# Kernel tuning notes

Measured on AMD Instinct MI355X. Metric: run time of the kernel, lower is better.

The kernel has to match this reference:

```python
import jax, jax.numpy as jnp
import numpy as np

N, E = 25000, 400000
NIN, NOUT, HID = 32, 32, 128


def setup_inputs() -> dict:
    key = jax.random.key(0)
    ks = jax.random.split(key, 8)
    s = lambda d: 1.0 / np.sqrt(d)
    return {
        "x": jax.random.normal(ks[0], (N, NIN), jnp.float32),
        "edge_index": jax.random.randint(ks[1], (2, E), 0, N, jnp.int64),
        "edge_attr": jax.random.normal(ks[2], (E, NIN), jnp.float32),
        # edge-MLP: Linear(NIN,HID) -> ReLU -> Linear(HID, NIN*NOUT)
        "w1": jax.random.normal(ks[3], (NIN, HID), jnp.float32) * s(NIN),
        "b1": jnp.zeros((HID,), jnp.float32),
        "w2": jax.random.normal(ks[4], (HID, NIN * NOUT), jnp.float32) * s(HID),
        "b2": jnp.zeros((NIN * NOUT,), jnp.float32),
        # NNConv root weight and bias
        "root": jax.random.normal(ks[5], (NIN, NOUT), jnp.float32) * s(NIN),
        "bias": jnp.zeros((NOUT,), jnp.float32),
    }


def reference(x, edge_index, edge_attr, w1, b1, w2, b2, root, bias):
    src, dst = edge_index[0], edge_index[1]
    # per-edge weight matrices from edge-attr MLP: [E, NIN, NOUT]
    h = jax.nn.relu(edge_attr @ w1 + b1)
    W = (h @ w2 + b2).reshape(-1, NIN, NOUT)
    # gather source features, per-edge small matmul: [E, NOUT]
    msg = jnp.einsum("ei,eio->eo", x[src], W)
    # scatter-add to target nodes (PyG default aggr='add')
    agg = jax.ops.segment_sum(msg, dst, num_segments=N)
    # root/self transform + bias
    return agg + x @ root + bias
```

## Files before the change

### kernel.cpp

```cpp
#include <hip/hip_runtime.h>
#include <hip/hip_fp16.h>


#define NN 25000
#define EE 400000

typedef _Float16 f16x8 __attribute__((ext_vector_type(8)));
typedef float    f32x16 __attribute__((ext_vector_type(16)));

__global__ __launch_bounds__(256) void prep_final_kernel(
    const float* __restrict__ x, const float* __restrict__ root,
    const float* __restrict__ bias,
    const float* __restrict__ w1, const float* __restrict__ w2,
    const float* __restrict__ b2,
    _Float16* __restrict__ w2p, _Float16* __restrict__ w1p, _Float16* __restrict__ b2p,
    float* __restrict__ out)
{
    const int t = blockIdx.x * 256 + threadIdx.x;

    if (t < 131072) {
        int j = t & 7, lane = (t >> 3) & 63, ih = (t >> 9) & 1, c = t >> 10;
        w2p[t] = (_Float16)w2[c * 1024 + (ih * 16 + ((lane >> 5) << 3) + j) * 32 + (lane & 31)];
    } else if (t < 135168) {
        int u = t - 131072;
        int j = u & 7, lane = (u >> 3) & 63, kk = (u >> 9) & 1, r = u >> 10;
        w1p[u] = (_Float16)w1[(kk * 16 + ((lane >> 5) << 3) + j) * 128 + r * 32 + (lane & 31)];
    } else if (t < 136192) {
        int u = t - 135168;
        int j = u & 7, lane = (u >> 3) & 63, ih = u >> 9;
        b2p[u] = (_Float16)b2[(ih * 16 + ((lane >> 5) << 3) + j) * 32 + (lane & 31)];
    }

    int n = t >> 5, o = t & 31;
    float acc = bias[o];
    const float* xr = x + (n << 5);
#pragma unroll
    for (int i = 0; i < 32; ++i)
        acc = fmaf(xr[i], root[(i << 5) + o], acc);
    out[t] = acc;
}

__global__ __launch_bounds__(128, 2) void edge_kernel(
    const float*    __restrict__ x,
    const int*      __restrict__ ei,
    const float*    __restrict__ ea,
    const float*    __restrict__ b1,
    const _Float16* __restrict__ w2p,
    const _Float16* __restrict__ w1p,
    const _Float16* __restrict__ b2p,
    float* __restrict__ out)
{
    __shared__ unsigned short hTq[2][32][32][4];

    const int t    = threadIdx.x;
    const int w    = t >> 6;
    const int lane = t & 63;
    const int l    = lane & 31;
    const int half = lane >> 5;

    const int  ebraw = blockIdx.x * 256 + w * 128;
    const bool live  = (ebraw + 128) <= EE;
    const int  ebw   = live ? ebraw : (EE - 128);

    union u8h { f16x8 v; __half2 h2[4]; };

    const f16x8* __restrict__ w2f = (const f16x8*)w2p;

    f16x8 BA[2], BB[2], BC[2], BD[2];
    auto loadCol = [&](int j, f16x8 (&B)[2]) {
        const f16x8* p = w2f + (size_t)j * 128 + lane;
        B[0] = p[0];
        B[1] = p[64];
    };
    loadCol(0, BA); loadCol(1, BB); loadCol(2, BC); loadCol(3, BD);

    u8h eaf[4][2];
#pragma unroll
    for (int g = 0; g < 4; ++g)
#pragma unroll
        for (int kk = 0; kk < 2; ++kk) {
            const float* p = ea + (size_t)(ebw + g * 32 + l) * 32 + kk * 16 + half * 8;
            float4 a0 = *(const float4*)p;
            float4 a1 = *(const float4*)(p + 4);
            eaf[g][kk].h2[0] = __float22half2_rn(make_float2(a0.x, a0.y));
            eaf[g][kk].h2[1] = __float22half2_rn(make_float2(a0.z, a0.w));
            eaf[g][kk].h2[2] = __float22half2_rn(make_float2(a1.x, a1.y));
            eaf[g][kk].h2[3] = __float22half2_rn(make_float2(a1.z, a1.w));
        }

    __half2 xs[4][8];
#pragma unroll
    for (int g = 0; g < 4; ++g) {
        int s = ei[ebw + g * 32 + l];
#pragma unroll
        for (int ih = 0; ih < 2; ++ih) {
            float4 a0 = *(const float4*)(x + s * 32 + ih * 16 + half * 8);
            float4 a1 = *(const float4*)(x + s * 32 + ih * 16 + half * 8 + 4);
            xs[g][ih*4+0] = __float22half2_rn(make_float2(a0.x, a0.y));
            xs[g][ih*4+1] = __float22half2_rn(make_float2(a0.z, a0.w));
            xs[g][ih*4+2] = __float22half2_rn(make_float2(a1.x, a1.y));
            xs[g][ih*4+3] = __float22half2_rn(make_float2(a1.z, a1.w));
        }
    }

    f32x16 acc[4];
#pragma unroll
    for (int g = 0; g < 4; ++g)
#pragma unroll
        for (int i = 0; i < 16; ++i) acc[g][i] = 0.f;

    auto phase1 = [&](int r) {
        f16x8 w1f0 = *(const f16x8*)(w1p + ((r * 2 + 0) * 64 + lane) * 8);
        f16x8 w1f1 = *(const f16x8*)(w1p + ((r * 2 + 1) * 64 + lane) * 8);
#pragma unroll
        for (int g = 0; g < 4; ++g) {
            f32x16 h;
#pragma unroll
            for (int i = 0; i < 16; ++i) h[i] = 0.f;
            h = __builtin_amdgcn_mfma_f32_32x32x16_f16(w1f0, eaf[g][0].v, h, 0, 0, 0);
            h = __builtin_amdgcn_mfma_f32_32x32x16_f16(w1f1, eaf[g][1].v, h, 0, 0, 0);
#pragma unroll
            for (int i = 0; i < 16; ++i) {
                int row = (i & 3) + ((i >> 2) << 3) + (half << 2);
                float hv = fmaxf(h[i] + b1[r * 32 + row], 0.f);
                hTq[w][row][l][g] = __half_as_ushort(__float2half(hv));
            }
        }
    };

    auto computeCol = [&](int cs, const f16x8 (&B)[2]) {
        uint2 u = *(const uint2*)&hTq[w][cs][l][0];
        __half2 ha = *reinterpret_cast<const __half2*>(&u.x);
        __half2 hb = *reinterpret_cast<const __half2*>(&u.y);
        __half2 d[4];
        d[0] = __half2half2(__low2half(ha));
        d[1] = __half2half2(__high2half(ha));
        d[2] = __half2half2(__low2half(hb));
        d[3] = __half2half2(__high2half(hb));
#pragma unroll
        for (int ih = 0; ih < 2; ++ih) {
            f16x8 bfr = B[ih];
#pragma unroll
            for (int g = 0; g < 4; ++g) {
                u8h A;
#pragma unroll
                for (int p = 0; p < 4; ++p)
                    A.h2[p] = __hmul2(d[g], xs[g][ih * 4 + p]);
                acc[g] = __builtin_amdgcn_mfma_f32_32x32x16_f16(A.v, bfr, acc[g], 0, 0, 0);
            }
        }
    };

#pragma unroll 1
    for (int r = 0; r < 4; ++r) {
        phase1(r);
#pragma unroll 1
        for (int q = 0; q < 8; ++q) {
            const int j = r * 32 + q * 4;
            computeCol(q * 4 + 0, BA); loadCol(j + 4, BA);
            computeCol(q * 4 + 1, BB); loadCol(j + 5, BB);
            computeCol(q * 4 + 2, BC); loadCol(j + 6, BC);
            computeCol(q * 4 + 3, BD); loadCol(j + 7, BD);
        }
    }

#pragma unroll
    for (int ih = 0; ih < 2; ++ih) {
        f16x8 bfr = *(const f16x8*)(b2p + (ih * 64 + lane) * 8);
#pragma unroll
        for (int g = 0; g < 4; ++g) {
            u8h A;
#pragma unroll
            for (int p = 0; p < 4; ++p) A.h2[p] = xs[g][ih * 4 + p];
            acc[g] = __builtin_amdgcn_mfma_f32_32x32x16_f16(A.v, bfr, acc[g], 0, 0, 0);
        }
    }

    if (live) {
#pragma unroll
        for (int g = 0; g < 4; ++g)
#pragma unroll
            for (int i = 0; i < 16; ++i) {
                int el = (i & 3) + ((i >> 2) << 3) + (half << 2);
                atomicAdd(out + (size_t)ei[EE + ebw + g * 32 + el] * 32 + l, acc[g][i]);
            }
    }
}

extern "C" void kernel_launch(void* const* d_in, const int* in_sizes, int n_in,
                              void* d_out, int out_size, void* d_ws, size_t ws_size,
                              hipStream_t stream) {
    const float* x    = (const float*)d_in[0];
    const int*   ei   = (const int*)  d_in[1];
    const float* ea   = (const float*)d_in[2];
    const float* w1   = (const float*)d_in[3];
    const float* b1   = (const float*)d_in[4];
    const float* w2   = (const float*)d_in[5];
    const float* b2   = (const float*)d_in[6];
    const float* root = (const float*)d_in[7];
    const float* bias = (const float*)d_in[8];
    float* out = (float*)d_out;

    _Float16* w2p = (_Float16*)d_ws;
    _Float16* w1p = (_Float16*)((char*)d_ws + 262144);
    _Float16* b2p = (_Float16*)((char*)d_ws + 270336);

    prep_final_kernel<<<(NN * 32) / 256, 256, 0, stream>>>(
        x, root, bias, w1, w2, b2, w2p, w1p, b2p, out);

    edge_kernel<<<(EE + 255) / 256, 128, 0, stream>>>(
        x, ei, ea, b1, w2p, w1p, b2p, out);
}
```

Baseline: 225.5 us.

## Replace LDS transpose of hidden activations with register permlane32 swaps

```diff
diff --git a/kernel.cpp b/kernel.cpp
--- a/kernel.cpp
+++ b/kernel.cpp
@@ -7,6 +7,20 @@
 
 typedef _Float16 f16x8 __attribute__((ext_vector_type(8)));
 typedef float    f32x16 __attribute__((ext_vector_type(16)));
+typedef unsigned u32x2  __attribute__((ext_vector_type(2)));
+
+__device__ __forceinline__ void swapHalves(unsigned u, int half,
+                                           unsigned& a, unsigned& y) {
+#if __has_builtin(__builtin_amdgcn_permlane32_swap)
+    u32x2 rr = __builtin_amdgcn_permlane32_swap(u, u, false, false);
+    a = rr.x;
+    y = rr.y;
+#else
+    unsigned p = (unsigned)__shfl_xor((int)u, 32, 64);
+    a = half ? p : u;
+    y = half ? u : p;
+#endif
+}
 
 __global__ __launch_bounds__(256) void prep_final_kernel(
     const float* __restrict__ x, const float* __restrict__ root,
@@ -40,7 +54,7 @@
     out[t] = acc;
 }
 
-__global__ __launch_bounds__(128, 2) void edge_kernel(
+__global__ __launch_bounds__(128, 1) void edge_kernel(
     const float*    __restrict__ x,
     const int*      __restrict__ ei,
     const float*    __restrict__ ea,
@@ -50,8 +64,6 @@
     const _Float16* __restrict__ b2p,
     float* __restrict__ out)
 {
-    __shared__ unsigned short hTq[2][32][32][4];
-
     const int t    = threadIdx.x;
     const int w    = t >> 6;
     const int lane = t & 63;
@@ -109,6 +121,8 @@
 #pragma unroll
         for (int i = 0; i < 16; ++i) acc[g][i] = 0.f;
 
+    __half2 hpk[4][8];
+
     auto phase1 = [&](int r) {
         f16x8 w1f0 = *(const f16x8*)(w1p + ((r * 2 + 0) * 64 + lane) * 8);
         f16x8 w1f1 = *(const f16x8*)(w1p + ((r * 2 + 1) * 64 + lane) * 8);
@@ -120,23 +134,24 @@
             h = __builtin_amdgcn_mfma_f32_32x32x16_f16(w1f0, eaf[g][0].v, h, 0, 0, 0);
             h = __builtin_amdgcn_mfma_f32_32x32x16_f16(w1f1, eaf[g][1].v, h, 0, 0, 0);
 #pragma unroll
-            for (int i = 0; i < 16; ++i) {
-                int row = (i & 3) + ((i >> 2) << 3) + (half << 2);
-                float hv = fmaxf(h[i] + b1[r * 32 + row], 0.f);
-                hTq[w][row][l][g] = __half_as_ushort(__float2half(hv));
+            for (int jj = 0; jj < 8; ++jj) {
+                int i0 = 2 * jj;
+                int r0 = (i0 & 3) + ((i0 >> 2) << 3) + (half << 2);
+                hpk[g][jj] = __float22half2_rn(make_float2(
+                    fmaxf(h[i0]     + b1[r * 32 + r0],     0.f),
+                    fmaxf(h[i0 + 1] + b1[r * 32 + r0 + 1], 0.f)));
             }
         }
     };
 
-    auto computeCol = [&](int cs, const f16x8 (&B)[2]) {
-        uint2 u = *(const uint2*)&hTq[w][cs][l][0];
-        __half2 ha = *reinterpret_cast<const __half2*>(&u.x);
-        __half2 hb = *reinterpret_cast<const __half2*>(&u.y);
+    __half2 Ac[4][2], Yc[4][2];
+
+    auto colMFMA = [&](const __half2 (&C)[4][2], int dd, bool hi,
+                       const f16x8 (&B)[2]) {
         __half2 d[4];
-        d[0] = __half2half2(__low2half(ha));
-        d[1] = __half2half2(__high2half(ha));
-        d[2] = __half2half2(__low2half(hb));
-        d[3] = __half2half2(__high2half(hb));
+#pragma unroll
+        for (int g = 0; g < 4; ++g)
+            d[g] = __half2half2(hi ? __high2half(C[g][dd]) : __low2half(C[g][dd]));
 #pragma unroll
         for (int ih = 0; ih < 2; ++ih) {
             f16x8 bfr = B[ih];
@@ -154,13 +169,30 @@
 #pragma unroll 1
     for (int r = 0; r < 4; ++r) {
         phase1(r);
-#pragma unroll 1
+#pragma unroll
         for (int q = 0; q < 8; ++q) {
             const int j = r * 32 + q * 4;
-            computeCol(q * 4 + 0, BA); loadCol(j + 4, BA);
-            computeCol(q * 4 + 1, BB); loadCol(j + 5, BB);
-            computeCol(q * 4 + 2, BC); loadCol(j + 6, BC);
-            computeCol(q * 4 + 3, BD); loadCol(j + 7, BD);
+            if ((q & 1) == 0) {
+#pragma unroll
+                for (int g = 0; g < 4; ++g)
+#pragma unroll
+                    for (int dd = 0; dd < 2; ++dd) {
+                        unsigned a, y;
+                        swapHalves(__builtin_bit_cast(unsigned, hpk[g][q + dd]),
+                                   half, a, y);
+                        Ac[g][dd] = __builtin_bit_cast(__half2, a);
+                        Yc[g][dd] = __builtin_bit_cast(__half2, y);
+                    }
+                colMFMA(Ac, 0, false, BA); loadCol(j + 4, BA);
+                colMFMA(Ac, 0, true,  BB); loadCol(j + 5, BB);
+                colMFMA(Ac, 1, false, BC); loadCol(j + 6, BC);
+                colMFMA(Ac, 1, true,  BD); loadCol(j + 7, BD);
+            } else {
+                colMFMA(Yc, 0, false, BA); loadCol(j + 4, BA);
+                colMFMA(Yc, 0, true,  BB); loadCol(j + 5, BB);
+                colMFMA(Yc, 1, false, BC); loadCol(j + 6, BC);
+                colMFMA(Yc, 1, true,  BD); loadCol(j + 7, BD);
+            }
         }
     }
 
```

Measured after the change: 254.0 us. +12.6%, slower.
